# Kernel tuning notes

Hardware: AMD Instinct MI355X
Metric: run time of the kernel (lower is better)

Reference implementation:

```python
import jax, jax.numpy as jnp
import numpy as np

N_NODES = 100000
N_EDGES = 2000000
D_IN = 4
HID = 64


def setup_inputs() -> dict:
    key = jax.random.key(0)
    ks = jax.random.split(key, 8)
    node_feats = jax.random.normal(ks[0], (N_NODES, D_IN), dtype=jnp.float32)
    pairs = jax.random.randint(ks[1], (N_EDGES, 2), 0, N_NODES, dtype=jnp.int64)
    # Kaiming-ish init scaling
    W1 = jax.random.normal(ks[2], (D_IN, HID), dtype=jnp.float32) / np.sqrt(D_IN)
    b1 = jnp.zeros((HID,), dtype=jnp.float32)
    W2 = jax.random.normal(ks[3], (HID, HID), dtype=jnp.float32) / np.sqrt(HID)
    b2 = jnp.zeros((HID,), dtype=jnp.float32)
    We1 = jax.random.normal(ks[4], (3 * HID, HID), dtype=jnp.float32) / np.sqrt(3 * HID)
    be1 = jnp.zeros((HID,), dtype=jnp.float32)
    We2 = jax.random.normal(ks[5], (HID, 1), dtype=jnp.float32) / np.sqrt(HID)
    be2 = jnp.zeros((1,), dtype=jnp.float32)
    return {"node_feats": node_feats, "pairs": pairs, "W1": W1, "b1": b1,
            "W2": W2, "b2": b2, "We1": We1, "be1": be1, "We2": We2, "be2": be2}


def reference(node_feats, pairs, W1, b1, W2, b2, We1, be1, We2, be2):
    # node MLP: Linear -> ReLU -> Linear -> ReLU
    H = jax.nn.relu(node_feats @ W1 + b1)      # [N, HID]
    H = jax.nn.relu(H @ W2 + b2)               # [N, HID]
    # vectorized gather over all edge pairs (replaces Python loop)
    hu = H[pairs[:, 0]]                        # [E, HID]
    hv = H[pairs[:, 1]]                        # [E, HID]
    E = jnp.concatenate([hu, hv, jnp.abs(hu - hv)], axis=-1)  # [E, 3*HID]
    # edge MLP: Linear -> ReLU -> Linear, squeeze last dim
    scores = (jax.nn.relu(E @ We1 + be1) @ We2 + be2)[:, 0]   # [E]
    return scores
```

## Files before the change

kernel.cpp:

```cpp
#include <hip/hip_runtime.h>

#define N_NODES 100000
#define N_EDGES 2000000

typedef __bf16 bf16x8 __attribute__((ext_vector_type(8)));
typedef float f32x4 __attribute__((ext_vector_type(4)));
typedef float f32x16 __attribute__((ext_vector_type(16)));

#define AS1 __attribute__((address_space(1)))
#define AS3 __attribute__((address_space(3)))

__device__ __forceinline__ unsigned f2bf_rne(float f) {
  unsigned u = __builtin_bit_cast(unsigned, f);
  u += 0x7FFFu + ((u >> 16) & 1u);
  return u >> 16;
}

__device__ __forceinline__ unsigned pack_rhu(float lo, float hi) {
  unsigned ulo = __builtin_bit_cast(unsigned, lo) + 0x8000u;
  unsigned uhi = __builtin_bit_cast(unsigned, hi) + 0x8000u;
  return __builtin_amdgcn_perm(uhi, ulo, 0x07060302u);
}

__device__ __forceinline__ unsigned absdiff_pack(unsigned a, unsigned b) {
  float alo = __builtin_bit_cast(float, a << 16);
  float ahi = __builtin_bit_cast(float, a & 0xFFFF0000u);
  float blo = __builtin_bit_cast(float, b << 16);
  float bhi = __builtin_bit_cast(float, b & 0xFFFF0000u);
  return pack_rhu(fabsf(alo - blo), fabsf(ahi - bhi));
}

__global__ __launch_bounds__(64, 1) void node_mfma_kernel(
    const float* __restrict__ X, const float* __restrict__ W1,
    const float* __restrict__ b1, const float* __restrict__ W2,
    const float* __restrict__ b2, unsigned short* __restrict__ H) {
  const int lane = threadIdx.x;
  const int l15 = lane & 15;
  const int quad = lane >> 4;

  float w1v[2][4][8], b1v[2][8];
#pragma unroll
  for (int c = 0; c < 2; ++c)
#pragma unroll
    for (int j = 0; j < 8; ++j) {
      int col = c * 32 + quad * 8 + j;
      b1v[c][j] = b1[col];
#pragma unroll
      for (int d = 0; d < 4; ++d) w1v[c][d][j] = W1[d * 64 + col];
    }

  uint4 afr[2][4];
#pragma unroll
  for (int c = 0; c < 2; ++c)
#pragma unroll
    for (int mt = 0; mt < 4; ++mt) {
      unsigned w[4];
#pragma unroll
      for (int p = 0; p < 4; ++p) {
        int k = c * 32 + quad * 8 + 2 * p;
        unsigned lo = f2bf_rne(W2[k * 64 + mt * 16 + l15]);
        unsigned hi = f2bf_rne(W2[(k + 1) * 64 + mt * 16 + l15]);
        w[p] = lo | (hi << 16);
      }
      afr[c][mt] = make_uint4(w[0], w[1], w[2], w[3]);
    }
  float b2v[16];
#pragma unroll
  for (int mt = 0; mt < 4; ++mt)
#pragma unroll
    for (int r = 0; r < 4; ++r) b2v[mt * 4 + r] = b2[mt * 16 + quad * 4 + r];

  const int ntiles = N_NODES / 16;
  for (int tile = blockIdx.x; tile < ntiles; tile += gridDim.x) {
    float4 xv = ((const float4*)X)[tile * 16 + l15];

    uint4 bfr[2];
#pragma unroll
    for (int c = 0; c < 2; ++c) {
      unsigned w[4];
#pragma unroll
      for (int p = 0; p < 4; ++p) {
        float h0 = fmaxf(b1v[c][2 * p] + xv.x * w1v[c][0][2 * p] +
                             xv.y * w1v[c][1][2 * p] + xv.z * w1v[c][2][2 * p] +
                             xv.w * w1v[c][3][2 * p],
                         0.f);
        float h1 = fmaxf(b1v[c][2 * p + 1] + xv.x * w1v[c][0][2 * p + 1] +
                             xv.y * w1v[c][1][2 * p + 1] +
                             xv.z * w1v[c][2][2 * p + 1] +
                             xv.w * w1v[c][3][2 * p + 1],
                         0.f);
        w[p] = pack_rhu(h0, h1);
      }
      bfr[c] = make_uint4(w[0], w[1], w[2], w[3]);
    }

    f32x4 acc[4];
#pragma unroll
    for (int mt = 0; mt < 4; ++mt) acc[mt] = (f32x4){0.f, 0.f, 0.f, 0.f};
#pragma unroll
    for (int c = 0; c < 2; ++c)
#pragma unroll
      for (int mt = 0; mt < 4; ++mt)
        acc[mt] = __builtin_amdgcn_mfma_f32_16x16x32_bf16(
            __builtin_bit_cast(bf16x8, afr[c][mt]),
            __builtin_bit_cast(bf16x8, bfr[c]), acc[mt], 0, 0, 0);

    unsigned short* hrow = H + (tile * 16 + l15) * 64;
#pragma unroll
    for (int mt = 0; mt < 4; ++mt) {
      unsigned lo = pack_rhu(fmaxf(acc[mt][0] + b2v[mt * 4 + 0], 0.f),
                             fmaxf(acc[mt][1] + b2v[mt * 4 + 1], 0.f));
      unsigned hi = pack_rhu(fmaxf(acc[mt][2] + b2v[mt * 4 + 2], 0.f),
                             fmaxf(acc[mt][3] + b2v[mt * 4 + 3], 0.f));
      *(uint2*)(hrow + mt * 16 + quad * 4) = make_uint2(lo, hi);
    }
  }
}

__global__ __launch_bounds__(256, 2) void edge_mlp_kernel(
    const unsigned short* __restrict__ H, const int* __restrict__ pairs,
    const float* __restrict__ We1, const float* __restrict__ be1,
    const float* __restrict__ We2, const float* __restrict__ be2,
    float* __restrict__ out) {
  __shared__ uint4 gbuf[4][2][512];
  __shared__ uint4 scratch[64];
  const int tid = threadIdx.x;
  const int lane = tid & 63;
  const int n = lane & 31;
  const int half = lane >> 5;
  const int wave = tid >> 6;
  const int rowsel = lane >> 3;
  const int swzc = (lane & 7) ^ rowsel;

  uint4 afr[13][2];
#pragma unroll
  for (int c = 0; c < 12; ++c)
#pragma unroll
    for (int mt = 0; mt < 2; ++mt) {
      int col = mt * 32 + n;
      int kb = c * 16 + half * 8;
      unsigned w[4];
#pragma unroll
      for (int p = 0; p < 4; ++p)
        w[p] = f2bf_rne(We1[(kb + 2 * p) * 64 + col]) |
               (f2bf_rne(We1[(kb + 2 * p + 1) * 64 + col]) << 16);
      afr[c][mt] = make_uint4(w[0], w[1], w[2], w[3]);
    }
#pragma unroll
  for (int mt = 0; mt < 2; ++mt)
    afr[12][mt] =
        make_uint4((half == 0) ? f2bf_rne(be1[mt * 32 + n]) : 0u, 0u, 0u, 0u);

  const uint4 b13u = make_uint4((half == 0) ? 0x00003F80u : 0u, 0u, 0u, 0u);

  float we2v[32];
#pragma unroll
  for (int mt = 0; mt < 2; ++mt)
#pragma unroll
    for (int r = 0; r < 16; ++r)
      we2v[mt * 16 + r] = We2[mt * 32 + (r & 3) + 8 * (r >> 2) + 4 * half];
  const float be2v = be2[0];

  uint4* const bufA = &gbuf[wave][0][0];
  uint4* const bufB = &gbuf[wave][1][0];
  int rbo[4];
#pragma unroll
  for (int c = 0; c < 4; ++c) rbo[c] = n * 8 + ((2 * c + half) ^ (n & 7));

  const int wid = blockIdx.x * 4 + wave;
  const int nw = gridDim.x * 4;
  const int ntiles = N_EDGES / 32;
  const int last = ntiles - 1;
  const int2* pairs2 = (const int2*)pairs;

  auto issue_gathers = [&](uint4* dst, const int2* prs) {
#pragma unroll
    for (int k = 0; k < 4; ++k) {
      const AS1 unsigned* gu =
          (const AS1 unsigned*)(H + (size_t)prs[k].x * 64) + swzc * 4;
      const AS1 unsigned* gv =
          (const AS1 unsigned*)(H + (size_t)prs[k].y * 64) + swzc * 4;
      __builtin_amdgcn_global_load_lds(gu, (AS3 unsigned*)(dst + k * 64), 16,
                                       0, 0);
      __builtin_amdgcn_global_load_lds(
          gv, (AS3 unsigned*)(dst + 256 + k * 64), 16, 0, 0);
    }
  };

  int2 pr[4];
  {
#pragma unroll
    for (int k = 0; k < 4; ++k) pr[k] = pairs2[wid * 32 + k * 8 + rowsel];
    issue_gathers(bufA, pr);
    int t1 = wid + nw <= last ? wid + nw : last;
#pragma unroll
    for (int k = 0; k < 4; ++k) pr[k] = pairs2[t1 * 32 + k * 8 + rowsel];
    __builtin_amdgcn_global_load_lds((const AS1 unsigned*)H,
                                     (AS3 unsigned*)scratch, 16, 0, 0);
  }

  auto body = [&](int tc, uint4* CONS, uint4* FILL) {
    __builtin_amdgcn_sched_barrier(0);
    __builtin_amdgcn_s_waitcnt(0x0F75);
    __builtin_amdgcn_sched_barrier(0);

    issue_gathers(FILL, pr);
    __builtin_amdgcn_sched_barrier(0);
    {
      int tn = tc + 2 * nw <= last ? tc + 2 * nw : last;
#pragma unroll
      for (int k = 0; k < 4; ++k) pr[k] = pairs2[tn * 32 + k * 8 + rowsel];
    }

    const int t = tc <= last ? tc : last;
    uint4 hu[4], hv[4];
#pragma unroll
    for (int c = 0; c < 4; ++c) {
      hu[c] = CONS[rbo[c]];
      hv[c] = CONS[256 + rbo[c]];
    }
    uint4 ab[4];
#pragma unroll
    for (int c = 0; c < 4; ++c) {
      ab[c].x = absdiff_pack(hu[c].x, hv[c].x);
      ab[c].y = absdiff_pack(hu[c].y, hv[c].y);
      ab[c].z = absdiff_pack(hu[c].z, hv[c].z);
      ab[c].w = absdiff_pack(hu[c].w, hv[c].w);
    }

    f32x16 acc[2];
    acc[0] = (f32x16)(0.f);
    acc[1] = (f32x16)(0.f);
#pragma unroll
    for (int c = 0; c < 13; ++c) {
      uint4 bu = (c < 4) ? hu[c]
                         : (c < 8) ? hv[c - 4] : (c < 12 ? ab[c - 8] : b13u);
      bf16x8 b = __builtin_bit_cast(bf16x8, bu);
#pragma unroll
      for (int mt = 0; mt < 2; ++mt)
        acc[mt] = __builtin_amdgcn_mfma_f32_32x32x16_bf16(
            __builtin_bit_cast(bf16x8, afr[c][mt]), b, acc[mt], 0, 0, 0);
    }

    float s = 0.f;
#pragma unroll
    for (int mt = 0; mt < 2; ++mt)
#pragma unroll
      for (int r = 0; r < 16; ++r)
        s += fmaxf(acc[mt][r], 0.f) * we2v[mt * 16 + r];
    s += __shfl_xor(s, 32);
    if (half == 0) out[t * 32 + n] = s + be2v;
  };

  for (int t = wid; t < ntiles; t += 2 * nw) {
    body(t, bufA, bufB);
    body(t + nw, bufB, bufA);
  }
}

extern "C" void kernel_launch(void* const* d_in, const int* in_sizes, int n_in,
                              void* d_out, int out_size, void* d_ws,
                              size_t ws_size, hipStream_t stream) {
  const float* X = (const float*)d_in[0];
  const int* pairs = (const int*)d_in[1];
  const float* W1 = (const float*)d_in[2];
  const float* b1 = (const float*)d_in[3];
  const float* W2 = (const float*)d_in[4];
  const float* b2 = (const float*)d_in[5];
  const float* We1 = (const float*)d_in[6];
  const float* be1 = (const float*)d_in[7];
  const float* We2 = (const float*)d_in[8];
  const float* be2 = (const float*)d_in[9];
  float* out = (float*)d_out;
  unsigned short* H = (unsigned short*)d_ws;

  node_mfma_kernel<<<1024, 64, 0, stream>>>(X, W1, b1, W2, b2, H);
  edge_mlp_kernel<<<512, 256, 0, stream>>>(H, pairs, We1, be1, We2, be2, out);
}
```

Measured before the change: 161.1 us.

## Replace LDS-staged gather with direct register loads prefetched mid-MFMA

```diff
diff --git a/kernel.cpp b/kernel.cpp
--- a/kernel.cpp
+++ b/kernel.cpp
@@ -6,9 +6,6 @@
 typedef __bf16 bf16x8 __attribute__((ext_vector_type(8)));
 typedef float f32x4 __attribute__((ext_vector_type(4)));
 typedef float f32x16 __attribute__((ext_vector_type(16)));
-
-#define AS1 __attribute__((address_space(1)))
-#define AS3 __attribute__((address_space(3)))
 
 __device__ __forceinline__ unsigned f2bf_rne(float f) {
   unsigned u = __builtin_bit_cast(unsigned, f);
@@ -122,15 +119,11 @@
     const float* __restrict__ We1, const float* __restrict__ be1,
     const float* __restrict__ We2, const float* __restrict__ be2,
     float* __restrict__ out) {
-  __shared__ uint4 gbuf[4][2][512];
-  __shared__ uint4 scratch[64];
   const int tid = threadIdx.x;
   const int lane = tid & 63;
   const int n = lane & 31;
   const int half = lane >> 5;
   const int wave = tid >> 6;
-  const int rowsel = lane >> 3;
-  const int swzc = (lane & 7) ^ rowsel;
 
   uint4 afr[13][2];
 #pragma unroll
@@ -160,12 +153,6 @@
     for (int r = 0; r < 16; ++r)
       we2v[mt * 16 + r] = We2[mt * 32 + (r & 3) + 8 * (r >> 2) + 4 * half];
   const float be2v = be2[0];
-
-  uint4* const bufA = &gbuf[wave][0][0];
-  uint4* const bufB = &gbuf[wave][1][0];
-  int rbo[4];
-#pragma unroll
-  for (int c = 0; c < 4; ++c) rbo[c] = n * 8 + ((2 * c + half) ^ (n & 7));
 
   const int wid = blockIdx.x * 4 + wave;
   const int nw = gridDim.x * 4;
@@ -173,52 +160,26 @@
   const int last = ntiles - 1;
   const int2* pairs2 = (const int2*)pairs;
 
-  auto issue_gathers = [&](uint4* dst, const int2* prs) {
-#pragma unroll
-    for (int k = 0; k < 4; ++k) {
-      const AS1 unsigned* gu =
-          (const AS1 unsigned*)(H + (size_t)prs[k].x * 64) + swzc * 4;
-      const AS1 unsigned* gv =
-          (const AS1 unsigned*)(H + (size_t)prs[k].y * 64) + swzc * 4;
-      __builtin_amdgcn_global_load_lds(gu, (AS3 unsigned*)(dst + k * 64), 16,
-                                       0, 0);
-      __builtin_amdgcn_global_load_lds(
-          gv, (AS3 unsigned*)(dst + 256 + k * 64), 16, 0, 0);
-    }
-  };
-
-  int2 pr[4];
+  const unsigned short* Hh = H + half * 8;
+
+  int2 pr = pairs2[(size_t)wid * 32 + n];
+  uint4 hu[4], hv[4];
   {
-#pragma unroll
-    for (int k = 0; k < 4; ++k) pr[k] = pairs2[wid * 32 + k * 8 + rowsel];
-    issue_gathers(bufA, pr);
-    int t1 = wid + nw <= last ? wid + nw : last;
-#pragma unroll
-    for (int k = 0; k < 4; ++k) pr[k] = pairs2[t1 * 32 + k * 8 + rowsel];
-    __builtin_amdgcn_global_load_lds((const AS1 unsigned*)H,
-                                     (AS3 unsigned*)scratch, 16, 0, 0);
-  }
-
-  auto body = [&](int tc, uint4* CONS, uint4* FILL) {
-    __builtin_amdgcn_sched_barrier(0);
-    __builtin_amdgcn_s_waitcnt(0x0F75);
-    __builtin_amdgcn_sched_barrier(0);
-
-    issue_gathers(FILL, pr);
-    __builtin_amdgcn_sched_barrier(0);
-    {
-      int tn = tc + 2 * nw <= last ? tc + 2 * nw : last;
-#pragma unroll
-      for (int k = 0; k < 4; ++k) pr[k] = pairs2[tn * 32 + k * 8 + rowsel];
-    }
-
-    const int t = tc <= last ? tc : last;
-    uint4 hu[4], hv[4];
-#pragma unroll
-    for (int c = 0; c < 4; ++c) {
-      hu[c] = CONS[rbo[c]];
-      hv[c] = CONS[256 + rbo[c]];
-    }
+    const uint4* pu = (const uint4*)(Hh + (size_t)pr.x * 64);
+    const uint4* pv = (const uint4*)(Hh + (size_t)pr.y * 64);
+#pragma unroll
+    for (int c = 0; c < 4; ++c) {
+      hu[c] = pu[2 * c];
+      hv[c] = pv[2 * c];
+    }
+  }
+  {
+    int t1 = wid + nw;
+    if (t1 > last) t1 = last;
+    pr = pairs2[(size_t)t1 * 32 + n];
+  }
+
+  for (int t = wid; t < ntiles; t += nw) {
     uint4 ab[4];
 #pragma unroll
     for (int c = 0; c < 4; ++c) {
@@ -231,16 +192,51 @@
     f32x16 acc[2];
     acc[0] = (f32x16)(0.f);
     acc[1] = (f32x16)(0.f);
-#pragma unroll
-    for (int c = 0; c < 13; ++c) {
-      uint4 bu = (c < 4) ? hu[c]
-                         : (c < 8) ? hv[c - 4] : (c < 12 ? ab[c - 8] : b13u);
-      bf16x8 b = __builtin_bit_cast(bf16x8, bu);
+
+#pragma unroll
+    for (int c = 0; c < 4; ++c) {
+      bf16x8 b = __builtin_bit_cast(bf16x8, hu[c]);
 #pragma unroll
       for (int mt = 0; mt < 2; ++mt)
         acc[mt] = __builtin_amdgcn_mfma_f32_32x32x16_bf16(
             __builtin_bit_cast(bf16x8, afr[c][mt]), b, acc[mt], 0, 0, 0);
     }
+#pragma unroll
+    for (int c = 0; c < 4; ++c) {
+      bf16x8 b = __builtin_bit_cast(bf16x8, hv[c]);
+#pragma unroll
+      for (int mt = 0; mt < 2; ++mt)
+        acc[mt] = __builtin_amdgcn_mfma_f32_32x32x16_bf16(
+            __builtin_bit_cast(bf16x8, afr[4 + c][mt]), b, acc[mt], 0, 0, 0);
+    }
+
+    {
+      const uint4* pu = (const uint4*)(Hh + (size_t)pr.x * 64);
+      const uint4* pv = (const uint4*)(Hh + (size_t)pr.y * 64);
+#pragma unroll
+      for (int c = 0; c < 4; ++c) {
+        hu[c] = pu[2 * c];
+        hv[c] = pv[2 * c];
+      }
+      int t2 = t + 2 * nw;
+      if (t2 > last) t2 = last;
+      pr = pairs2[(size_t)t2 * 32 + n];
+    }
+    __builtin_amdgcn_sched_barrier(0);
+
+#pragma unroll
+    for (int c = 0; c < 4; ++c) {
+      bf16x8 b = __builtin_bit_cast(bf16x8, ab[c]);
+#pragma unroll
+      for (int mt = 0; mt < 2; ++mt)
+        acc[mt] = __builtin_amdgcn_mfma_f32_32x32x16_bf16(
+            __builtin_bit_cast(bf16x8, afr[8 + c][mt]), b, acc[mt], 0, 0, 0);
+    }
+#pragma unroll
+    for (int mt = 0; mt < 2; ++mt)
+      acc[mt] = __builtin_amdgcn_mfma_f32_32x32x16_bf16(
+          __builtin_bit_cast(bf16x8, afr[12][mt]),
+          __builtin_bit_cast(bf16x8, b13u), acc[mt], 0, 0, 0);
 
     float s = 0.f;
 #pragma unroll
@@ -250,11 +246,6 @@
         s += fmaxf(acc[mt][r], 0.f) * we2v[mt * 16 + r];
     s += __shfl_xor(s, 32);
     if (half == 0) out[t * 32 + n] = s + be2v;
-  };
-
-  for (int t = wid; t < ntiles; t += 2 * nw) {
-    body(t, bufA, bufB);
-    body(t + nw, bufB, bufA);
   }
 }
 
```

After: 175.0 us. 1.09x slower.
